# Kernel optimization log

Hardware: AMD Instinct MI355X
Metric: run time of the kernel (lower is better)

Reference implementation:

```python
import jax, jax.numpy as jnp
import numpy as np

N_NODES = 100000


def _gcn_layer(x, W, b, src, dst, edge_weight):
    # GCNConv with normalize=False: linear transform, then weighted scatter-add
    h = x @ W                                   # [N, out]
    msg = h[src] * edge_weight[:, None]         # gather source features, scale per edge
    agg = jax.ops.segment_sum(msg, dst, num_segments=N_NODES)  # scatter-add to destinations
    return agg + b


def setup_inputs() -> dict:
    key = jax.random.key(0)
    k = jax.random.split(key, 6)
    N, F_in, H, C, E = N_NODES, 256, 16, 40, 3200000
    x = jax.random.normal(k[0], (N, F_in), dtype=jnp.float32)
    edge_index = jax.random.randint(k[1], (2, E), 0, N, dtype=jnp.int64)
    edge_weight = jax.random.uniform(k[2], (E,), dtype=jnp.float32)
    # Glorot-style init for weights
    W1 = jax.random.normal(k[3], (F_in, H), dtype=jnp.float32) * (1.0 / np.sqrt(F_in))
    b1 = jnp.zeros((H,), dtype=jnp.float32)
    W2 = jax.random.normal(k[4], (H, C), dtype=jnp.float32) * (1.0 / np.sqrt(H))
    b2 = jnp.zeros((C,), dtype=jnp.float32)
    return {"x": x, "edge_index": edge_index, "edge_weight": edge_weight,
            "W1": W1, "b1": b1, "W2": W2, "b2": b2}


def reference(x, edge_index, edge_weight, W1, b1, W2, b2):
    src, dst = edge_index[0], edge_index[1]
    h = jax.nn.relu(_gcn_layer(x, W1, b1, src, dst, edge_weight))
    # dropout is identity in eval mode
    h = _gcn_layer(h, W2, b2, src, dst, edge_weight)
    return jax.nn.log_softmax(h, axis=1)
```

## Files before the change

### kernel.cpp

```cpp
#include <hip/hip_runtime.h>
#include <hip/hip_bf16.h>
#include <cstdint>

#define F_IN 256
#define F_H  16
#define F_P  8
#define F_C  40
#define XS   32

__global__ __launch_bounds__(256) void gemm1_kernel(
    const float* __restrict__ x, const float* __restrict__ W1,
    __hip_bfloat162* __restrict__ t1, int N) {
  __shared__ float xlds[XS * 260];
  __shared__ float wlds[F_H * 260];
  const int tid = threadIdx.x;
  const int nodeBase = blockIdx.x * XS;

  for (int i = tid; i < F_IN * F_H; i += 256) {
    int k = i >> 4, f = i & 15;
    wlds[f * 260 + k] = W1[i];
  }
  const float4* x4 = reinterpret_cast<const float4*>(x) + (size_t)nodeBase * (F_IN / 4);
  for (int i = tid; i < XS * (F_IN / 4); i += 256) {
    int r = i >> 6, c4 = i & 63;
    float4 v = make_float4(0.f, 0.f, 0.f, 0.f);
    if (nodeBase + r < N) v = x4[(size_t)r * (F_IN / 4) + c4];
    *reinterpret_cast<float4*>(&xlds[r * 260 + c4 * 4]) = v;
  }
  __syncthreads();

  const int r0 = tid >> 4;
  const int f  = tid & 15;
  const float4* xa = reinterpret_cast<const float4*>(&xlds[r0 * 260]);
  const float4* xb = reinterpret_cast<const float4*>(&xlds[(r0 + 16) * 260]);
  const float4* wf = reinterpret_cast<const float4*>(&wlds[f * 260]);
  float acca = 0.f, accb = 0.f;
#pragma unroll 8
  for (int k4 = 0; k4 < F_IN / 4; ++k4) {
    float4 w = wf[k4];
    float4 a = xa[k4];
    float4 b = xb[k4];
    acca = fmaf(a.x, w.x, acca); acca = fmaf(a.y, w.y, acca);
    acca = fmaf(a.z, w.z, acca); acca = fmaf(a.w, w.w, acca);
    accb = fmaf(b.x, w.x, accb); accb = fmaf(b.y, w.y, accb);
    accb = fmaf(b.z, w.z, accb); accb = fmaf(b.w, w.w, accb);
  }

  float hia = __shfl_down(acca, 1);
  float hib = __shfl_down(accb, 1);
  if ((f & 1) == 0) {
    int p = f >> 1;
    if (nodeBase + r0 < N)
      t1[(size_t)(nodeBase + r0) * F_P + p] =
          __halves2bfloat162(__float2bfloat16(acca), __float2bfloat16(hia));
    if (nodeBase + r0 + 16 < N)
      t1[(size_t)(nodeBase + r0 + 16) * F_P + p] =
          __halves2bfloat162(__float2bfloat16(accb), __float2bfloat16(hib));
  }
}

__global__ __launch_bounds__(256) void scatter1_kernel(
    const __hip_bfloat162* __restrict__ t1, const int* __restrict__ ei,
    const float* __restrict__ ew, __hip_bfloat162* __restrict__ agg1,
    int N, int E) {
  int gid = blockIdx.x * 256 + threadIdx.x;
  int e = gid >> 3;
  int p = gid & 7;
  if (e >= E) return;
  int s = ei[e];
  int d = ei[E + e];
  if ((unsigned)s >= (unsigned)N || (unsigned)d >= (unsigned)N) return;
  float w = ew[e];
  __hip_bfloat162 tv = t1[(size_t)s * F_P + p];
  __hip_bfloat162 v = __halves2bfloat162(
      __float2bfloat16(__bfloat162float(tv.x) * w),
      __float2bfloat16(__bfloat162float(tv.y) * w));
  unsafeAtomicAdd(&agg1[(size_t)d * F_P + p], v);
}

__global__ __launch_bounds__(256) void scatter2_kernel(
    const __hip_bfloat162* __restrict__ agg1, const float* __restrict__ b1,
    const int* __restrict__ ei, const float* __restrict__ ew,
    __hip_bfloat162* __restrict__ agg2, int N, int E) {
  int gid = blockIdx.x * 256 + threadIdx.x;
  int e = gid >> 3;
  int p = gid & 7;
  if (e >= E) return;
  int s = ei[e];
  int d = ei[E + e];
  if ((unsigned)s >= (unsigned)N || (unsigned)d >= (unsigned)N) return;
  float w = ew[e];
  __hip_bfloat162 av = agg1[(size_t)s * F_P + p];
  float lo = __bfloat162float(av.x) + b1[2 * p];
  float hi = __bfloat162float(av.y) + b1[2 * p + 1];
  lo = lo > 0.f ? lo * w : 0.f;
  hi = hi > 0.f ? hi * w : 0.f;
  __hip_bfloat162 v = __halves2bfloat162(__float2bfloat16(lo), __float2bfloat16(hi));
  unsafeAtomicAdd(&agg2[(size_t)d * F_P + p], v);
}

__global__ __launch_bounds__(320) void gemm2_lsm_kernel(
    const __hip_bfloat162* __restrict__ agg2, const float* __restrict__ W2,
    const float* __restrict__ b2, float* __restrict__ out, int N) {
  __shared__ float w2lds[F_H * F_C];
  __shared__ float alds[8 * F_H];
  __shared__ float slds[8 * F_C];
  __shared__ float mlog[8];
  const int tid = threadIdx.x;
  const int nodeBase = blockIdx.x * 8;

  for (int i = tid; i < F_H * F_C; i += 320) w2lds[i] = W2[i];
  if (tid < 8 * F_P) {
    int node = nodeBase + (tid >> 3);
    __hip_bfloat162 v{};
    if (node < N) v = agg2[(size_t)nodeBase * F_P + tid];
    int r = tid >> 3, p = tid & 7;
    alds[r * F_H + 2 * p]     = __bfloat162float(v.x);
    alds[r * F_H + 2 * p + 1] = __bfloat162float(v.y);
  }
  __syncthreads();

  const int ln = tid / F_C;
  const int c = tid - ln * F_C;
  float acc = b2[c];
#pragma unroll
  for (int k = 0; k < F_H; ++k) acc = fmaf(alds[ln * F_H + k], w2lds[k * F_C + c], acc);
  slds[tid] = acc;
  __syncthreads();

  if (tid < 8) {
    const float* row = &slds[tid * F_C];
    float m = -INFINITY;
#pragma unroll
    for (int f = 0; f < F_C; ++f) m = fmaxf(m, row[f]);
    float s = 0.f;
#pragma unroll
    for (int f = 0; f < F_C; ++f) s += expf(row[f] - m);
    mlog[tid] = m + logf(s);
  }
  __syncthreads();

  const int node = nodeBase + ln;
  if (node < N) out[(size_t)nodeBase * F_C + tid] = slds[tid] - mlog[ln];
}

extern "C" void kernel_launch(void* const* d_in, const int* in_sizes, int n_in,
                              void* d_out, int out_size, void* d_ws, size_t ws_size,
                              hipStream_t stream) {
  const float* x  = (const float*)d_in[0];
  const int*   ei = (const int*)d_in[1];
  const float* ew = (const float*)d_in[2];
  const float* W1 = (const float*)d_in[3];
  const float* b1 = (const float*)d_in[4];
  const float* W2 = (const float*)d_in[5];
  const float* b2 = (const float*)d_in[6];
  float* out = (float*)d_out;

  const int N = in_sizes[0] / F_IN;
  const int E = in_sizes[2];

  __hip_bfloat162* t1   = (__hip_bfloat162*)d_ws;
  __hip_bfloat162* agg1 = t1 + (size_t)N * F_P;
  __hip_bfloat162* agg2 = agg1 + (size_t)N * F_P;

  hipMemsetAsync(agg1, 0, (size_t)N * F_P * 2 * sizeof(__hip_bfloat162), stream);

  gemm1_kernel<<<(N + XS - 1) / XS, 256, 0, stream>>>(x, W1, t1, N);
  scatter1_kernel<<<((size_t)E * F_P + 255) / 256, 256, 0, stream>>>(t1, ei, ew, agg1, N, E);
  scatter2_kernel<<<((size_t)E * F_P + 255) / 256, 256, 0, stream>>>(agg1, b1, ei, ew, agg2, N, E);
  gemm2_lsm_kernel<<<(N + 7) / 8, 320, 0, stream>>>(agg2, W2, b2, out, N);
}
```

Measured before the change: 550.2 us.

## Fold memset into gemm1, process two edges per thread, and restructure log-softmax

The separate hipMemsetAsync is removed and the agg1/agg2 buffers are zeroed inside gemm1. Both scatter kernels now handle two edges per thread with the gathers hoisted before the atomics, halving the thread count and exposing more memory-level parallelism. The final GEMM+log-softmax kernel is rewritten so that 32 nodes per block use 8 threads each, computing 5 classes per thread with shuffle reductions and fast exp/log, which removes the single-thread serial softmax and extra barriers. The fast intrinsics may slightly change numerics.

```diff
diff --git a/kernel.cpp b/kernel.cpp
--- a/kernel.cpp
+++ b/kernel.cpp
@@ -10,11 +10,18 @@
 
 __global__ __launch_bounds__(256) void gemm1_kernel(
     const float* __restrict__ x, const float* __restrict__ W1,
-    __hip_bfloat162* __restrict__ t1, int N) {
+    __hip_bfloat162* __restrict__ t1,
+    unsigned* __restrict__ agg1z, unsigned* __restrict__ agg2z, int N) {
   __shared__ float xlds[XS * 260];
   __shared__ float wlds[F_H * 260];
   const int tid = threadIdx.x;
   const int nodeBase = blockIdx.x * XS;
+
+  {
+    int lim = min(XS, N - nodeBase) * F_P;
+    size_t base = (size_t)nodeBase * F_P;
+    if (tid < lim) { agg1z[base + tid] = 0u; agg2z[base + tid] = 0u; }
+  }
 
   for (int i = tid; i < F_IN * F_H; i += 256) {
     int k = i >> 4, f = i & 15;
@@ -64,18 +71,35 @@
     const float* __restrict__ ew, __hip_bfloat162* __restrict__ agg1,
     int N, int E) {
   int gid = blockIdx.x * 256 + threadIdx.x;
-  int e = gid >> 3;
   int p = gid & 7;
-  if (e >= E) return;
-  int s = ei[e];
-  int d = ei[E + e];
-  if ((unsigned)s >= (unsigned)N || (unsigned)d >= (unsigned)N) return;
-  float w = ew[e];
-  __hip_bfloat162 tv = t1[(size_t)s * F_P + p];
-  __hip_bfloat162 v = __halves2bfloat162(
-      __float2bfloat16(__bfloat162float(tv.x) * w),
-      __float2bfloat16(__bfloat162float(tv.y) * w));
-  unsafeAtomicAdd(&agg1[(size_t)d * F_P + p], v);
+  int e0 = (gid >> 3) << 1;
+  if (e0 >= E) return;
+  int e1 = e0 + 1;
+  bool ok1 = (e1 < E);
+
+  int s0 = ei[e0], d0 = ei[E + e0];
+  int s1 = ok1 ? ei[e1] : s0;
+  int d1 = ok1 ? ei[E + e1] : d0;
+  float w0 = ew[e0];
+  float w1 = ok1 ? ew[e1] : 0.f;
+
+  bool v0 = ((unsigned)s0 < (unsigned)N) && ((unsigned)d0 < (unsigned)N);
+  bool v1 = ok1 && ((unsigned)s1 < (unsigned)N) && ((unsigned)d1 < (unsigned)N);
+  __hip_bfloat162 t0 = t1[(size_t)(v0 ? s0 : 0) * F_P + p];
+  __hip_bfloat162 t1v = t1[(size_t)(v1 ? s1 : 0) * F_P + p];
+
+  if (v0) {
+    __hip_bfloat162 a = __halves2bfloat162(
+        __float2bfloat16(__bfloat162float(t0.x) * w0),
+        __float2bfloat16(__bfloat162float(t0.y) * w0));
+    unsafeAtomicAdd(&agg1[(size_t)d0 * F_P + p], a);
+  }
+  if (v1) {
+    __hip_bfloat162 a = __halves2bfloat162(
+        __float2bfloat16(__bfloat162float(t1v.x) * w1),
+        __float2bfloat16(__bfloat162float(t1v.y) * w1));
+    unsafeAtomicAdd(&agg1[(size_t)d1 * F_P + p], a);
+  }
 }
 
 __global__ __launch_bounds__(256) void scatter2_kernel(
@@ -83,65 +107,91 @@
     const int* __restrict__ ei, const float* __restrict__ ew,
     __hip_bfloat162* __restrict__ agg2, int N, int E) {
   int gid = blockIdx.x * 256 + threadIdx.x;
-  int e = gid >> 3;
   int p = gid & 7;
-  if (e >= E) return;
-  int s = ei[e];
-  int d = ei[E + e];
-  if ((unsigned)s >= (unsigned)N || (unsigned)d >= (unsigned)N) return;
-  float w = ew[e];
-  __hip_bfloat162 av = agg1[(size_t)s * F_P + p];
-  float lo = __bfloat162float(av.x) + b1[2 * p];
-  float hi = __bfloat162float(av.y) + b1[2 * p + 1];
-  lo = lo > 0.f ? lo * w : 0.f;
-  hi = hi > 0.f ? hi * w : 0.f;
-  __hip_bfloat162 v = __halves2bfloat162(__float2bfloat16(lo), __float2bfloat16(hi));
-  unsafeAtomicAdd(&agg2[(size_t)d * F_P + p], v);
-}
-
-__global__ __launch_bounds__(320) void gemm2_lsm_kernel(
+  int e0 = (gid >> 3) << 1;
+  if (e0 >= E) return;
+  int e1 = e0 + 1;
+  bool ok1 = (e1 < E);
+
+  float2 bb = reinterpret_cast<const float2*>(b1)[p];
+  int s0 = ei[e0], d0 = ei[E + e0];
+  int s1 = ok1 ? ei[e1] : s0;
+  int d1 = ok1 ? ei[E + e1] : d0;
+  float w0 = ew[e0];
+  float w1 = ok1 ? ew[e1] : 0.f;
+
+  bool v0 = ((unsigned)s0 < (unsigned)N) && ((unsigned)d0 < (unsigned)N);
+  bool v1 = ok1 && ((unsigned)s1 < (unsigned)N) && ((unsigned)d1 < (unsigned)N);
+  __hip_bfloat162 a0 = agg1[(size_t)(v0 ? s0 : 0) * F_P + p];
+  __hip_bfloat162 a1 = agg1[(size_t)(v1 ? s1 : 0) * F_P + p];
+
+  if (v0) {
+    float lo = fmaxf(__bfloat162float(a0.x) + bb.x, 0.f) * w0;
+    float hi = fmaxf(__bfloat162float(a0.y) + bb.y, 0.f) * w0;
+    unsafeAtomicAdd(&agg2[(size_t)d0 * F_P + p],
+                    __halves2bfloat162(__float2bfloat16(lo), __float2bfloat16(hi)));
+  }
+  if (v1) {
+    float lo = fmaxf(__bfloat162float(a1.x) + bb.x, 0.f) * w1;
+    float hi = fmaxf(__bfloat162float(a1.y) + bb.y, 0.f) * w1;
+    unsafeAtomicAdd(&agg2[(size_t)d1 * F_P + p],
+                    __halves2bfloat162(__float2bfloat16(lo), __float2bfloat16(hi)));
+  }
+}
+
+__global__ __launch_bounds__(256) void gemm2_lsm_kernel(
     const __hip_bfloat162* __restrict__ agg2, const float* __restrict__ W2,
     const float* __restrict__ b2, float* __restrict__ out, int N) {
   __shared__ float w2lds[F_H * F_C];
-  __shared__ float alds[8 * F_H];
-  __shared__ float slds[8 * F_C];
-  __shared__ float mlog[8];
+  __shared__ float b2lds[F_C];
+  __shared__ float alds[XS * F_H];
   const int tid = threadIdx.x;
-  const int nodeBase = blockIdx.x * 8;
-
-  for (int i = tid; i < F_H * F_C; i += 320) w2lds[i] = W2[i];
-  if (tid < 8 * F_P) {
+  const int nodeBase = blockIdx.x * XS;
+
+  for (int i = tid; i < F_H * F_C; i += 256) w2lds[i] = W2[i];
+  if (tid < F_C) b2lds[tid] = b2[tid];
+  {
     int node = nodeBase + (tid >> 3);
-    __hip_bfloat162 v{};
-    if (node < N) v = agg2[(size_t)nodeBase * F_P + tid];
-    int r = tid >> 3, p = tid & 7;
-    alds[r * F_H + 2 * p]     = __bfloat162float(v.x);
-    alds[r * F_H + 2 * p + 1] = __bfloat162float(v.y);
+    __hip_bfloat162 v = __halves2bfloat162(__float2bfloat16(0.f), __float2bfloat16(0.f));
+    if (node < N) v = agg2[(size_t)node * F_P + (tid & 7)];
+    alds[(tid >> 3) * F_H + 2 * (tid & 7)]     = __bfloat162float(v.x);
+    alds[(tid >> 3) * F_H + 2 * (tid & 7) + 1] = __bfloat162float(v.y);
   }
   __syncthreads();
 
-  const int ln = tid / F_C;
-  const int c = tid - ln * F_C;
-  float acc = b2[c];
-#pragma unroll
-  for (int k = 0; k < F_H; ++k) acc = fmaf(alds[ln * F_H + k], w2lds[k * F_C + c], acc);
-  slds[tid] = acc;
-  __syncthreads();
-
-  if (tid < 8) {
-    const float* row = &slds[tid * F_C];
-    float m = -INFINITY;
-#pragma unroll
-    for (int f = 0; f < F_C; ++f) m = fmaxf(m, row[f]);
-    float s = 0.f;
-#pragma unroll
-    for (int f = 0; f < F_C; ++f) s += expf(row[f] - m);
-    mlog[tid] = m + logf(s);
-  }
-  __syncthreads();
-
-  const int node = nodeBase + ln;
-  if (node < N) out[(size_t)nodeBase * F_C + tid] = slds[tid] - mlog[ln];
+  const int r = tid >> 3;
+  const int l = tid & 7;
+  const int node = nodeBase + r;
+  const float* arow = &alds[r * F_H];
+
+  float acc[5];
+#pragma unroll
+  for (int j = 0; j < 5; ++j) {
+    int c = l * 5 + j;
+    float a = b2lds[c];
+#pragma unroll
+    for (int k = 0; k < F_H; ++k) a = fmaf(arow[k], w2lds[k * F_C + c], a);
+    acc[j] = a;
+  }
+
+  float m = acc[0];
+#pragma unroll
+  for (int j = 1; j < 5; ++j) m = fmaxf(m, acc[j]);
+#pragma unroll
+  for (int off = 1; off < 8; off <<= 1) m = fmaxf(m, __shfl_xor(m, off, 8));
+
+  float s = 0.f;
+#pragma unroll
+  for (int j = 0; j < 5; ++j) s += __expf(acc[j] - m);
+#pragma unroll
+  for (int off = 1; off < 8; off <<= 1) s += __shfl_xor(s, off, 8);
+
+  float ml = m + __logf(s);
+  if (node < N) {
+#pragma unroll
+    for (int j = 0; j < 5; ++j)
+      out[(size_t)node * F_C + l * 5 + j] = acc[j] - ml;
+  }
 }
 
 extern "C" void kernel_launch(void* const* d_in, const int* in_sizes, int n_in,
@@ -163,10 +213,9 @@
   __hip_bfloat162* agg1 = t1 + (size_t)N * F_P;
   __hip_bfloat162* agg2 = agg1 + (size_t)N * F_P;
 
-  hipMemsetAsync(agg1, 0, (size_t)N * F_P * 2 * sizeof(__hip_bfloat162), stream);
-
-  gemm1_kernel<<<(N + XS - 1) / XS, 256, 0, stream>>>(x, W1, t1, N);
-  scatter1_kernel<<<((size_t)E * F_P + 255) / 256, 256, 0, stream>>>(t1, ei, ew, agg1, N, E);
-  scatter2_kernel<<<((size_t)E * F_P + 255) / 256, 256, 0, stream>>>(agg1, b1, ei, ew, agg2, N, E);
-  gemm2_lsm_kernel<<<(N + 7) / 8, 320, 0, stream>>>(agg2, W2, b2, out, N);
-}
+  gemm1_kernel<<<(N + XS - 1) / XS, 256, 0, stream>>>(
+      x, W1, t1, (unsigned*)agg1, (unsigned*)agg2, N);
+  scatter1_kernel<<<((size_t)E * 4 + 255) / 256, 256, 0, stream>>>(t1, ei, ew, agg1, N, E);
+  scatter2_kernel<<<((size_t)E * 4 + 255) / 256, 256, 0, stream>>>(agg1, b1, ei, ew, agg2, N, E);
+  gemm2_lsm_kernel<<<(N + XS - 1) / XS, 256, 0, stream>>>(agg2, W2, b2, out, N);
+}
```

Measured after the change: 532.9 us. 1.03x faster.
